# Kernel optimization log

Hardware: AMD Instinct MI355X
Metric: run time of the kernel (lower is better)

## Reference

```python
import jax, jax.numpy as jnp
import numpy as np

B, S, D = 2, 2048, 512
H, DK, DV = 8, 64, 64
TEMP = DK ** 0.5


def setup_inputs() -> dict:
    key = jax.random.key(0)
    ks = jax.random.split(key, 12)
    inp = {
        "q": jax.random.normal(ks[0], (B, S, D), dtype=jnp.float32),
        "k": jax.random.normal(ks[1], (B, S, D), dtype=jnp.float32),
        "v": jax.random.normal(ks[2], (B, S, D), dtype=jnp.float32),
        "static_cov": jax.random.normal(ks[3], (B, S, S), dtype=jnp.float32),
        "mask": jax.random.randint(ks[4], (B, S, S), 0, 2, dtype=jnp.int32),
        # learned params (torch Linear(bias=False) weight is [out,in]; we store [in,out])
        "w_q": jax.random.normal(ks[5], (D, H * DK), dtype=jnp.float32) / np.sqrt(D),
        "w_k": jax.random.normal(ks[6], (D, H * DK), dtype=jnp.float32) / np.sqrt(D),
        "w_v": jax.random.normal(ks[7], (D, H * DV), dtype=jnp.float32) / np.sqrt(D),
        "w_fc": jax.random.normal(ks[8], (H * DV, D), dtype=jnp.float32) / np.sqrt(H * DV),
        "lambda_w": 10.0 * jnp.ones((1, H, 1, 1), dtype=jnp.float32),
        "ln_gamma": jnp.ones((D,), dtype=jnp.float32),
        "ln_beta": jnp.zeros((D,), dtype=jnp.float32),
    }
    return inp


def reference(q, k, v, static_cov, mask, w_q, w_k, w_v, w_fc, lambda_w, ln_gamma, ln_beta):
    residual = q
    # LayerNorm(eps=1e-6) on q only
    mu = jnp.mean(q, axis=-1, keepdims=True)
    var = jnp.mean(jnp.square(q - mu), axis=-1, keepdims=True)
    qn = (q - mu) / jnp.sqrt(var + 1e-6) * ln_gamma + ln_beta
    # projections -> [B, H, S, d]
    qh = (qn @ w_q).reshape(B, S, H, DK).transpose(0, 2, 1, 3)
    kh = (k @ w_k).reshape(B, S, H, DK).transpose(0, 2, 1, 3)
    vh = (v @ w_v).reshape(B, S, H, DV).transpose(0, 2, 1, 3)
    # convex blend of QK^T and static bias
    scores = jnp.einsum('bhqd,bhkd->bhqk', qh / TEMP, kh)  # [B,H,S,S]
    attn = scores / (lambda_w + 1.0) + (lambda_w / (lambda_w + 1.0)) * static_cov[:, None]
    attn = jnp.where(mask[:, None] == 0, -1e9, attn)
    attn = jax.nn.softmax(attn, axis=-1)
    out = jnp.einsum('bhqk,bhkd->bhqd', attn, vh)
    out = out.transpose(0, 2, 1, 3).reshape(B, S, H * DV)
    out = out @ w_fc + residual
    return (out, attn)
```

## Files before the change

kernel.cpp:

```cpp
#include <hip/hip_runtime.h>
#include <hip/hip_bf16.h>

typedef __attribute__((ext_vector_type(4))) float f32x4;
typedef __attribute__((ext_vector_type(4))) int i32x4;
typedef __attribute__((ext_vector_type(4))) unsigned int u32x4;
typedef __attribute__((ext_vector_type(8))) __bf16 bf16x8;

#define SDIM 2048
#define DDIM 512
#define HH 8
#define DH 64

static __device__ __forceinline__ f32x4 mfma_raw(bf16x8 a, bf16x8 b, f32x4 c) {
  return __builtin_amdgcn_mfma_f32_16x16x32_bf16(a, b, c, 0, 0, 0);
}

template <bool C1>
static __device__ __forceinline__ f32x4 mf(bf16x8 a, bf16x8 b, f32x4 c) {
  return C1 ? mfma_raw(a, b, c) : mfma_raw(b, a, c);
}

static __device__ __forceinline__ unsigned pack_bf16(float a, float b) {
  __bf16 x = (__bf16)a, y = (__bf16)b;
  unsigned short ux = __builtin_bit_cast(unsigned short, x);
  unsigned short uy = __builtin_bit_cast(unsigned short, y);
  return ((unsigned)uy << 16) | (unsigned)ux;
}

__global__ __launch_bounds__(256) void covm_kernel(const float* __restrict__ cov,
                                                   const int* __restrict__ mask,
                                                   float* __restrict__ covm,
                                                   int* __restrict__ flag) {
  if (blockIdx.x == 0 && threadIdx.x < 64) {
    float av = (float)(threadIdx.x & 15);
    float bv = av * av;
    bf16x8 a, b;
#pragma unroll
    for (int i = 0; i < 8; ++i) { a[i] = (__bf16)av; b[i] = (__bf16)bv; }
    f32x4 d = {};
    d = mfma_raw(a, b, d);
    if (threadIdx.x == 17) *flag = (d[0] == 128.0f) ? 1 : 2;
  }
  size_t i = ((size_t)blockIdx.x * 256 + threadIdx.x) * 4;
  f32x4 c = *(const f32x4*)(cov + i);
  i32x4 m = *(const i32x4*)(mask + i);
  f32x4 o;
#pragma unroll
  for (int r = 0; r < 4; ++r) o[r] = (m[r] == 0) ? -1e38f : c[r];
  *(f32x4*)(covm + i) = o;
}

__global__ __launch_bounds__(256) void ln_kernel(const float* __restrict__ q,
                                                 const float* __restrict__ gamma,
                                                 const float* __restrict__ beta,
                                                 __bf16* __restrict__ qn) {
  int row = blockIdx.x * 4 + (threadIdx.x >> 6);
  int lane = threadIdx.x & 63;
  const float* qr = q + (size_t)row * DDIM + lane * 8;
  f32x4 x0 = *(const f32x4*)qr;
  f32x4 x1 = *(const f32x4*)(qr + 4);
  float s = 0.f;
#pragma unroll
  for (int i = 0; i < 4; ++i) s += x0[i] + x1[i];
#pragma unroll
  for (int off = 32; off; off >>= 1) s += __shfl_xor(s, off);
  float mu = s * (1.f / DDIM);
  float vs = 0.f;
#pragma unroll
  for (int i = 0; i < 4; ++i) {
    float d0 = x0[i] - mu, d1 = x1[i] - mu;
    vs += d0 * d0 + d1 * d1;
  }
#pragma unroll
  for (int off = 32; off; off >>= 1) vs += __shfl_xor(vs, off);
  float inv = rsqrtf(vs * (1.f / DDIM) + 1e-6f);
  const float* g = gamma + lane * 8;
  const float* be = beta + lane * 8;
  bf16x8 o;
#pragma unroll
  for (int i = 0; i < 8; ++i) {
    float xv = (i < 4) ? x0[i] : x1[i - 4];
    o[i] = (__bf16)((xv - mu) * inv * g[i] + be[i]);
  }
  *(bf16x8*)(qn + (size_t)row * DDIM + lane * 8) = o;
}

__global__ __launch_bounds__(256) void wtrans_kernel(const float* __restrict__ w0,
                                                     const float* __restrict__ w1,
                                                     const float* __restrict__ w2,
                                                     const float* __restrict__ w3,
                                                     __bf16* __restrict__ t0,
                                                     __bf16* __restrict__ t1,
                                                     __bf16* __restrict__ t2,
                                                     __bf16* __restrict__ t3) {
  __shared__ float tile[64][65];
  const float* w = blockIdx.z == 0 ? w0 : blockIdx.z == 1 ? w1 : blockIdx.z == 2 ? w2 : w3;
  __bf16* t = blockIdx.z == 0 ? t0 : blockIdx.z == 1 ? t1 : blockIdx.z == 2 ? t2 : t3;
  int k0 = blockIdx.y * 64;
  int n0 = blockIdx.x * 64;
  int tx = threadIdx.x & 63, ty = threadIdx.x >> 6;
#pragma unroll
  for (int j = 0; j < 16; ++j) {
    int kk = ty * 16 + j;
    tile[kk][tx] = w[(size_t)(k0 + kk) * DDIM + n0 + tx];
  }
  __syncthreads();
#pragma unroll
  for (int j = 0; j < 16; ++j) {
    int n = ty * 16 + j;
    t[(size_t)(n0 + n) * DDIM + k0 + tx] = (__bf16)tile[tx][n];
  }
}

template <bool C1>
static __device__ __forceinline__ void proj_body(const __bf16* __restrict__ qn,
                                                 const float* __restrict__ kin,
                                                 const float* __restrict__ vin,
                                                 const __bf16* __restrict__ wqT,
                                                 const __bf16* __restrict__ wkT,
                                                 const __bf16* __restrict__ wvT,
                                                 const float* __restrict__ lam,
                                                 __bf16* __restrict__ qh,
                                                 __bf16* __restrict__ kh,
                                                 __bf16* __restrict__ vT,
                                                 __bf16* __restrict__ tr) {
  int which = blockIdx.z;
  int n0 = blockIdx.x * 64;
  int m0 = blockIdx.y * 64;
  int wid = threadIdx.x >> 6, lane = threadIdx.x & 63;
  int lr = lane & 15, lg = lane >> 4;
  int mrow = m0 + wid * 16;
  const __bf16* wT = which == 0 ? wqT : which == 1 ? wkT : wvT;
  f32x4 acc[4] = {};
  for (int kb = 0; kb < DDIM; kb += 32) {
    bf16x8 afrag;
    if (which == 0) {
      afrag = *(const bf16x8*)(qn + (size_t)(mrow + lr) * DDIM + kb + lg * 8);
    } else {
      const float* src = (which == 1 ? kin : vin) + (size_t)(mrow + lr) * DDIM + kb + lg * 8;
      f32x4 y0 = *(const f32x4*)src;
      f32x4 y1 = *(const f32x4*)(src + 4);
#pragma unroll
      for (int i = 0; i < 4; ++i) { afrag[i] = (__bf16)y0[i]; afrag[i + 4] = (__bf16)y1[i]; }
    }
#pragma unroll
    for (int c = 0; c < 4; ++c) {
      bf16x8 bfrag = *(const bf16x8*)(wT + (size_t)(n0 + c * 16 + lr) * DDIM + kb + lg * 8);
      acc[c] = mf<C1>(afrag, bfrag, acc[c]);
    }
  }
  int h = n0 >> 6;
  int bq = m0 >> 11;
  int ss0 = m0 & 2047;
  if (which == 0) {
    float sc = 1.f / (8.f * (lam[h] + 1.f));
#pragma unroll
    for (int c = 0; c < 4; ++c)
#pragma unroll
      for (int r = 0; r < 4; ++r)
        tr[(wid * 16 + lg * 4 + r) * 72 + c * 16 + lr] = (__bf16)(acc[c][r] * sc);
  } else if (which == 1) {
#pragma unroll
    for (int c = 0; c < 4; ++c)
#pragma unroll
      for (int r = 0; r < 4; ++r)
        tr[(wid * 16 + lg * 4 + r) * 72 + c * 16 + lr] = (__bf16)acc[c][r];
  } else {
#pragma unroll
    for (int c = 0; c < 4; ++c)
#pragma unroll
      for (int r = 0; r < 4; ++r)
        tr[(c * 16 + lr) * 72 + wid * 16 + lg * 4 + r] = (__bf16)acc[c][r];
  }
  __syncthreads();
  size_t bh2 = (size_t)bq * HH + h;
#pragma unroll
  for (int ii = 0; ii < 2; ++ii) {
    int row = (threadIdx.x >> 3) + ii * 32;
    int col = (threadIdx.x & 7) * 8;
    bf16x8 v8 = *(const bf16x8*)(tr + row * 72 + col);
    if (which == 2) {
      *(bf16x8*)(vT + (bh2 * DH + row) * SDIM + ss0 + col) = v8;
    } else {
      __bf16* dst = (which == 0 ? qh : kh);
      *(bf16x8*)(dst + (bh2 * SDIM + ss0 + row) * DH + col) = v8;
    }
  }
}

__global__ __launch_bounds__(256) void proj_kernel(const __bf16* __restrict__ qn,
                                                   const float* __restrict__ kin,
                                                   const float* __restrict__ vin,
                                                   const __bf16* __restrict__ wqT,
                                                   const __bf16* __restrict__ wkT,
                                                   const __bf16* __restrict__ wvT,
                                                   const float* __restrict__ lam,
                                                   __bf16* __restrict__ qh,
                                                   __bf16* __restrict__ kh,
                                                   __bf16* __restrict__ vT,
                                                   const int* __restrict__ flag) {
  extern __shared__ __bf16 psm[];
  if (*flag == 1) proj_body<true>(qn, kin, vin, wqT, wkT, wvT, lam, qh, kh, vT, psm);
  else            proj_body<false>(qn, kin, vin, wqT, wkT, wvT, lam, qh, kh, vT, psm);
}

template <bool C1>
static __device__ __forceinline__ void fused_body(const __bf16* __restrict__ qh,
                                                  const __bf16* __restrict__ kh,
                                                  const __bf16* __restrict__ vT,
                                                  const float* __restrict__ covm,
                                                  const float* __restrict__ lam,
                                                  float* __restrict__ attn,
                                                  __bf16* __restrict__ oh,
                                                  float* __restrict__ smem) {
  float* part  = smem;
  float* wredm = smem + 16 * 64 * 17;
  float* wreds = wredm + 256;
  int bid = blockIdx.x;
  int xcd = bid & 7;
  int seq = bid >> 3;
  int bh  = xcd * 2 + (seq & 1);
  int q0  = (seq >> 1) * 16;
  int b = bh >> 3, h = bh & 7;
  int wid = threadIdx.x >> 6, lane = threadIdx.x & 63;
  int lr = lane & 15, lg = lane >> 4;
  int col0 = wid * 128;
  const __bf16* qbase = qh + ((size_t)bh * SDIM + q0) * DH;
  const __bf16* kbase = kh + (size_t)bh * SDIM * DH;
  bf16x8 qf0 = *(const bf16x8*)(qbase + lr * DH + lg * 8);
  bf16x8 qf1 = *(const bf16x8*)(qbase + lr * DH + 32 + lg * 8);
  f32x4 acc[8];
#pragma unroll
  for (int c = 0; c < 8; ++c) {
    const __bf16* kp = kbase + (size_t)(col0 + c * 16 + lr) * DH + lg * 8;
    bf16x8 k0 = *(const bf16x8*)kp;
    bf16x8 k1 = *(const bf16x8*)(kp + 32);
    f32x4 t = {};
    t = mf<C1>(k0, qf0, t);
    t = mf<C1>(k1, qf1, t);
    acc[c] = t;
  }
  float blend = lam[h] / (lam[h] + 1.f);
  const float* crow = covm + ((size_t)b * SDIM + q0 + lr) * SDIM + col0 + lg * 4;
  float mx = -3.4e38f;
#pragma unroll
  for (int c = 0; c < 8; ++c) {
    f32x4 cv = *(const f32x4*)(crow + c * 16);
#pragma unroll
    for (int r = 0; r < 4; ++r) {
      float valv = acc[c][r] + blend * cv[r];
      valv = (cv[r] < -1e30f) ? -1e9f : valv;
      acc[c][r] = valv;
      mx = fmaxf(mx, valv);
    }
  }
  mx = fmaxf(mx, __shfl_xor(mx, 16));
  mx = fmaxf(mx, __shfl_xor(mx, 32));
  if (lg == 0) wredm[wid * 16 + lr] = mx;
  __syncthreads();
  float fm = wredm[lr];
#pragma unroll
  for (int w = 1; w < 16; ++w) fm = fmaxf(fm, wredm[w * 16 + lr]);
  float sm = 0.f;
#pragma unroll
  for (int c = 0; c < 8; ++c) {
#pragma unroll
    for (int r = 0; r < 4; ++r) {
      float p = __expf(acc[c][r] - fm);
      acc[c][r] = p;
      sm += p;
    }
  }
  sm += __shfl_xor(sm, 16);
  sm += __shfl_xor(sm, 32);
  if (lg == 0) wreds[wid * 16 + lr] = sm;
  __syncthreads();
  float ssum = wreds[lr];
#pragma unroll
  for (int w = 1; w < 16; ++w) ssum += wreds[w * 16 + lr];
  float inv = 1.f / ssum;
  unsigned pw[8][2];
#pragma unroll
  for (int c = 0; c < 8; ++c) {
    pw[c][0] = pack_bf16(acc[c][0] * inv, acc[c][1] * inv);
    pw[c][1] = pack_bf16(acc[c][2] * inv, acc[c][3] * inv);
  }
  const __bf16* vbase = vT + (size_t)bh * DH * SDIM + col0;
  int src0 = lr + 32 * (lg & 1);
  int src1 = src0 + 16;
  bool hi = (lg & 2) != 0;
  f32x4 oacc[4] = {};
#pragma unroll
  for (int t = 0; t < 4; ++t) {
    unsigned a0 = (unsigned)__shfl((int)pw[t * 2][0], src0);
    unsigned a1 = (unsigned)__shfl((int)pw[t * 2][1], src0);
    unsigned b0 = (unsigned)__shfl((int)pw[t * 2 + 1][0], src0);
    unsigned b1 = (unsigned)__shfl((int)pw[t * 2 + 1][1], src0);
    unsigned a2 = (unsigned)__shfl((int)pw[t * 2][0], src1);
    unsigned a3 = (unsigned)__shfl((int)pw[t * 2][1], src1);
    unsigned b2 = (unsigned)__shfl((int)pw[t * 2 + 1][0], src1);
    unsigned b3 = (unsigned)__shfl((int)pw[t * 2 + 1][1], src1);
    u32x4 wv;
    wv[0] = hi ? b0 : a0;
    wv[1] = hi ? b1 : a1;
    wv[2] = hi ? b2 : a2;
    wv[3] = hi ? b3 : a3;
    bf16x8 pfrag = __builtin_bit_cast(bf16x8, wv);
#pragma unroll
    for (int cp = 0; cp < 4; ++cp) {
      bf16x8 vfrag = *(const bf16x8*)(vbase + (size_t)(cp * 16 + lr) * SDIM + t * 32 + lg * 8);
      oacc[cp] = mf<C1>(vfrag, pfrag, oacc[cp]);
    }
  }
#pragma unroll
  for (int cp = 0; cp < 4; ++cp)
#pragma unroll
    for (int rp = 0; rp < 4; ++rp)
      part[(wid * 64 + cp * 16 + lg * 4 + rp) * 17 + lr] = oacc[cp][rp];
  __syncthreads();
  float* abase = attn + ((size_t)bh * SDIM + q0 + lr) * SDIM + col0 + lg * 4;
#pragma unroll
  for (int c = 0; c < 8; ++c) {
    f32x4 pn;
#pragma unroll
    for (int r = 0; r < 4; ++r) pn[r] = acc[c][r] * inv;
    *(f32x4*)(abase + c * 16) = pn;
  }
  {
    int qq = threadIdx.x >> 6;
    int dv = threadIdx.x & 63;
    float s = 0.f;
#pragma unroll
    for (int w = 0; w < 16; ++w) s += part[(w * 64 + dv) * 17 + qq];
    float sn = __shfl_xor(s, 1);
    if ((dv & 1) == 0) {
      unsigned ow = pack_bf16(s, sn);
      *(unsigned*)(oh + ((size_t)(b * SDIM + q0 + qq)) * DDIM + h * DH + dv) = ow;
    }
  }
}

__global__ __launch_bounds__(1024, 4) void fused_kernel_cov(const __bf16* __restrict__ qh,
                                                            const __bf16* __restrict__ kh,
                                                            const __bf16* __restrict__ vT,
                                                            const float* __restrict__ covm,
                                                            const float* __restrict__ lam,
                                                            float* __restrict__ attn,
                                                            __bf16* __restrict__ oh,
                                                            const int* __restrict__ flag) {
  extern __shared__ float smem[];
  if (*flag == 1) fused_body<true>(qh, kh, vT, covm, lam, attn, oh, smem);
  else            fused_body<false>(qh, kh, vT, covm, lam, attn, oh, smem);
}

template <bool C1>
static __device__ __forceinline__ void fc_body(const __bf16* __restrict__ oh,
                                               const __bf16* __restrict__ wfcT,
                                               const float* __restrict__ resid,
                                               float* __restrict__ out) {
  int n0 = blockIdx.x * 64;
  int m0 = blockIdx.y * 64;
  int wid = threadIdx.x >> 6, lane = threadIdx.x & 63;
  int lr = lane & 15, lg = lane >> 4;
  int mrow = m0 + wid * 16;
  f32x4 acc[4] = {};
  for (int kb = 0; kb < DDIM; kb += 32) {
    bf16x8 afrag = *(const bf16x8*)(oh + (size_t)(mrow + lr) * DDIM + kb + lg * 8);
#pragma unroll
    for (int c = 0; c < 4; ++c) {
      bf16x8 bfrag = *(const bf16x8*)(wfcT + (size_t)(n0 + c * 16 + lr) * DDIM + kb + lg * 8);
      acc[c] = mf<C1>(afrag, bfrag, acc[c]);
    }
  }
#pragma unroll
  for (int c = 0; c < 4; ++c)
#pragma unroll
    for (int r = 0; r < 4; ++r) {
      size_t m = mrow + lg * 4 + r;
      size_t n = n0 + c * 16 + lr;
      out[m * DDIM + n] = acc[c][r] + resid[m * DDIM + n];
    }
}

__global__ __launch_bounds__(256) void fc_kernel(const __bf16* __restrict__ oh,
                                                 const __bf16* __restrict__ wfcT,
                                                 const float* __restrict__ resid,
                                                 float* __restrict__ out,
                                                 const int* __restrict__ flag) {
  if (*flag == 1) fc_body<true>(oh, wfcT, resid, out);
  else            fc_body<false>(oh, wfcT, resid, out);
}

extern "C" void kernel_launch(void* const* d_in, const int* in_sizes, int n_in,
                              void* d_out, int out_size, void* d_ws, size_t ws_size,
                              hipStream_t stream) {
  const float* q = (const float*)d_in[0];
  const float* k = (const float*)d_in[1];
  const float* v = (const float*)d_in[2];
  const float* static_cov = (const float*)d_in[3];
  const int* mask = (const int*)d_in[4];
  const float* w_q = (const float*)d_in[5];
  const float* w_k = (const float*)d_in[6];
  const float* w_v = (const float*)d_in[7];
  const float* w_fc = (const float*)d_in[8];
  const float* lam = (const float*)d_in[9];
  const float* gamma = (const float*)d_in[10];
  const float* beta = (const float*)d_in[11];

  float* out = (float*)d_out;
  float* attn = out + (size_t)2 * SDIM * DDIM;

  char* ws = (char*)d_ws;
  const size_t MB4 = (size_t)4 << 20;
  __bf16* qn  = (__bf16*)(ws);
  __bf16* qh  = (__bf16*)(ws + 1 * MB4);
  __bf16* kh  = (__bf16*)(ws + 2 * MB4);
  __bf16* vT  = (__bf16*)(ws + 3 * MB4);
  __bf16* oh  = (__bf16*)(ws + 4 * MB4);
  __bf16* wqT = (__bf16*)(ws + 5 * MB4);
  __bf16* wkT = (__bf16*)(ws + 5 * MB4 + 524288);
  __bf16* wvT = (__bf16*)(ws + 5 * MB4 + 2 * 524288);
  __bf16* wfcT= (__bf16*)(ws + 5 * MB4 + 3 * 524288);
  int* flag   = (int*)(ws + 5 * MB4 + 4 * 524288);
  float* covm = (float*)(ws + 6 * MB4);

  const unsigned fused_smem = (16 * 64 * 17 + 256 + 256) * 4;
  const unsigned proj_smem  = 64 * 72 * 2;

  covm_kernel<<<dim3(2 * SDIM * SDIM / 1024), dim3(256), 0, stream>>>(static_cov, mask, covm, flag);
  ln_kernel<<<dim3(1024), dim3(256), 0, stream>>>(q, gamma, beta, qn);
  wtrans_kernel<<<dim3(8, 8, 4), dim3(256), 0, stream>>>(w_q, w_k, w_v, w_fc, wqT, wkT, wvT, wfcT);
  proj_kernel<<<dim3(8, 64, 3), dim3(256), proj_smem, stream>>>(qn, k, v, wqT, wkT, wvT, lam, qh, kh, vT, flag);
  fused_kernel_cov<<<dim3(2048), dim3(1024), fused_smem, stream>>>(qh, kh, vT, covm, lam, attn, oh, flag);
  fc_kernel<<<dim3(8, 64), dim3(256), 0, stream>>>(oh, wfcT, q, out, flag);
}
```

Before: 318.6 us.

## Merge prep kernels into one launch and use single-barrier softmax reduction

Result: faster. 311.5 us (-2.2%).

```diff
diff --git a/kernel.cpp b/kernel.cpp
--- a/kernel.cpp
+++ b/kernel.cpp
@@ -27,77 +27,84 @@
   return ((unsigned)uy << 16) | (unsigned)ux;
 }
 
-__global__ __launch_bounds__(256) void covm_kernel(const float* __restrict__ cov,
-                                                   const int* __restrict__ mask,
-                                                   float* __restrict__ covm,
-                                                   int* __restrict__ flag) {
-  if (blockIdx.x == 0 && threadIdx.x < 64) {
-    float av = (float)(threadIdx.x & 15);
-    float bv = av * av;
-    bf16x8 a, b;
-#pragma unroll
-    for (int i = 0; i < 8; ++i) { a[i] = (__bf16)av; b[i] = (__bf16)bv; }
-    f32x4 d = {};
-    d = mfma_raw(a, b, d);
-    if (threadIdx.x == 17) *flag = (d[0] == 128.0f) ? 1 : 2;
-  }
-  size_t i = ((size_t)blockIdx.x * 256 + threadIdx.x) * 4;
-  f32x4 c = *(const f32x4*)(cov + i);
-  i32x4 m = *(const i32x4*)(mask + i);
-  f32x4 o;
-#pragma unroll
-  for (int r = 0; r < 4; ++r) o[r] = (m[r] == 0) ? -1e38f : c[r];
-  *(f32x4*)(covm + i) = o;
-}
-
-__global__ __launch_bounds__(256) void ln_kernel(const float* __restrict__ q,
-                                                 const float* __restrict__ gamma,
-                                                 const float* __restrict__ beta,
-                                                 __bf16* __restrict__ qn) {
-  int row = blockIdx.x * 4 + (threadIdx.x >> 6);
-  int lane = threadIdx.x & 63;
-  const float* qr = q + (size_t)row * DDIM + lane * 8;
-  f32x4 x0 = *(const f32x4*)qr;
-  f32x4 x1 = *(const f32x4*)(qr + 4);
-  float s = 0.f;
-#pragma unroll
-  for (int i = 0; i < 4; ++i) s += x0[i] + x1[i];
-#pragma unroll
-  for (int off = 32; off; off >>= 1) s += __shfl_xor(s, off);
-  float mu = s * (1.f / DDIM);
-  float vs = 0.f;
-#pragma unroll
-  for (int i = 0; i < 4; ++i) {
-    float d0 = x0[i] - mu, d1 = x1[i] - mu;
-    vs += d0 * d0 + d1 * d1;
-  }
-#pragma unroll
-  for (int off = 32; off; off >>= 1) vs += __shfl_xor(vs, off);
-  float inv = rsqrtf(vs * (1.f / DDIM) + 1e-6f);
-  const float* g = gamma + lane * 8;
-  const float* be = beta + lane * 8;
-  bf16x8 o;
-#pragma unroll
-  for (int i = 0; i < 8; ++i) {
-    float xv = (i < 4) ? x0[i] : x1[i - 4];
-    o[i] = (__bf16)((xv - mu) * inv * g[i] + be[i]);
-  }
-  *(bf16x8*)(qn + (size_t)row * DDIM + lane * 8) = o;
-}
-
-__global__ __launch_bounds__(256) void wtrans_kernel(const float* __restrict__ w0,
+__global__ __launch_bounds__(256) void stageA_kernel(const float* __restrict__ cov,
+                                                     const int* __restrict__ mask,
+                                                     float* __restrict__ covm,
+                                                     const float* __restrict__ q,
+                                                     const float* __restrict__ gamma,
+                                                     const float* __restrict__ beta,
+                                                     __bf16* __restrict__ qn,
+                                                     const float* __restrict__ w0,
                                                      const float* __restrict__ w1,
                                                      const float* __restrict__ w2,
                                                      const float* __restrict__ w3,
                                                      __bf16* __restrict__ t0,
                                                      __bf16* __restrict__ t1,
                                                      __bf16* __restrict__ t2,
-                                                     __bf16* __restrict__ t3) {
+                                                     __bf16* __restrict__ t3,
+                                                     int* __restrict__ flag) {
   __shared__ float tile[64][65];
-  const float* w = blockIdx.z == 0 ? w0 : blockIdx.z == 1 ? w1 : blockIdx.z == 2 ? w2 : w3;
-  __bf16* t = blockIdx.z == 0 ? t0 : blockIdx.z == 1 ? t1 : blockIdx.z == 2 ? t2 : t3;
-  int k0 = blockIdx.y * 64;
-  int n0 = blockIdx.x * 64;
+  int bid = blockIdx.x;
+  if (bid < 8192) {
+    size_t i = ((size_t)bid * 256 + threadIdx.x) * 4;
+    f32x4 c = *(const f32x4*)(cov + i);
+    i32x4 m = *(const i32x4*)(mask + i);
+    f32x4 o;
+#pragma unroll
+    for (int r = 0; r < 4; ++r) o[r] = (m[r] == 0) ? -1e38f : c[r];
+    *(f32x4*)(covm + i) = o;
+    return;
+  }
+  if (bid < 9216) {
+    int lb = bid - 8192;
+    if (lb == 0 && threadIdx.x < 64) {
+      float av = (float)(threadIdx.x & 15);
+      float bv = av * av;
+      bf16x8 a, b;
+#pragma unroll
+      for (int i = 0; i < 8; ++i) { a[i] = (__bf16)av; b[i] = (__bf16)bv; }
+      f32x4 d = {};
+      d = mfma_raw(a, b, d);
+      if (threadIdx.x == 17) *flag = (d[0] == 128.0f) ? 1 : 2;
+    }
+    int row = lb * 4 + (threadIdx.x >> 6);
+    int lane = threadIdx.x & 63;
+    const float* qr = q + (size_t)row * DDIM + lane * 8;
+    f32x4 x0 = *(const f32x4*)qr;
+    f32x4 x1 = *(const f32x4*)(qr + 4);
+    float s = 0.f;
+#pragma unroll
+    for (int i = 0; i < 4; ++i) s += x0[i] + x1[i];
+#pragma unroll
+    for (int off = 32; off; off >>= 1) s += __shfl_xor(s, off);
+    float mu = s * (1.f / DDIM);
+    float vs = 0.f;
+#pragma unroll
+    for (int i = 0; i < 4; ++i) {
+      float d0 = x0[i] - mu, d1 = x1[i] - mu;
+      vs += d0 * d0 + d1 * d1;
+    }
+#pragma unroll
+    for (int off = 32; off; off >>= 1) vs += __shfl_xor(vs, off);
+    float inv = rsqrtf(vs * (1.f / DDIM) + 1e-6f);
+    const float* g = gamma + lane * 8;
+    const float* be = beta + lane * 8;
+    bf16x8 o;
+#pragma unroll
+    for (int i = 0; i < 8; ++i) {
+      float xv = (i < 4) ? x0[i] : x1[i - 4];
+      o[i] = (__bf16)((xv - mu) * inv * g[i] + be[i]);
+    }
+    *(bf16x8*)(qn + (size_t)row * DDIM + lane * 8) = o;
+    return;
+  }
+  int wb = bid - 9216;
+  int which = wb >> 6;
+  int rem = wb & 63;
+  int n0 = (rem & 7) * 64;
+  int k0 = (rem >> 3) * 64;
+  const float* w = which == 0 ? w0 : which == 1 ? w1 : which == 2 ? w2 : w3;
+  __bf16* t = which == 0 ? t0 : which == 1 ? t1 : which == 2 ? t2 : t3;
   int tx = threadIdx.x & 63, ty = threadIdx.x >> 6;
 #pragma unroll
   for (int j = 0; j < 16; ++j) {
@@ -256,34 +263,35 @@
   }
   mx = fmaxf(mx, __shfl_xor(mx, 16));
   mx = fmaxf(mx, __shfl_xor(mx, 32));
-  if (lg == 0) wredm[wid * 16 + lr] = mx;
-  __syncthreads();
-  float fm = wredm[lr];
-#pragma unroll
-  for (int w = 1; w < 16; ++w) fm = fmaxf(fm, wredm[w * 16 + lr]);
   float sm = 0.f;
 #pragma unroll
   for (int c = 0; c < 8; ++c) {
 #pragma unroll
     for (int r = 0; r < 4; ++r) {
-      float p = __expf(acc[c][r] - fm);
+      float p = __expf(acc[c][r] - mx);
       acc[c][r] = p;
       sm += p;
     }
   }
   sm += __shfl_xor(sm, 16);
   sm += __shfl_xor(sm, 32);
-  if (lg == 0) wreds[wid * 16 + lr] = sm;
+  if (lg == 0) {
+    wredm[wid * 16 + lr] = mx;
+    wreds[wid * 16 + lr] = sm;
+  }
   __syncthreads();
-  float ssum = wreds[lr];
-#pragma unroll
-  for (int w = 1; w < 16; ++w) ssum += wreds[w * 16 + lr];
-  float inv = 1.f / ssum;
+  float M = wredm[lr];
+#pragma unroll
+  for (int w = 1; w < 16; ++w) M = fmaxf(M, wredm[w * 16 + lr]);
+  float denom = 0.f;
+#pragma unroll
+  for (int w = 0; w < 16; ++w) denom += wreds[w * 16 + lr] * __expf(wredm[w * 16 + lr] - M);
+  float sc = __expf(mx - M) / denom;
   unsigned pw[8][2];
 #pragma unroll
   for (int c = 0; c < 8; ++c) {
-    pw[c][0] = pack_bf16(acc[c][0] * inv, acc[c][1] * inv);
-    pw[c][1] = pack_bf16(acc[c][2] * inv, acc[c][3] * inv);
+    pw[c][0] = pack_bf16(acc[c][0] * sc, acc[c][1] * sc);
+    pw[c][1] = pack_bf16(acc[c][2] * sc, acc[c][3] * sc);
   }
   const __bf16* vbase = vT + (size_t)bh * DH * SDIM + col0;
   int src0 = lr + 32 * (lg & 1);
@@ -323,7 +331,7 @@
   for (int c = 0; c < 8; ++c) {
     f32x4 pn;
 #pragma unroll
-    for (int r = 0; r < 4; ++r) pn[r] = acc[c][r] * inv;
+    for (int r = 0; r < 4; ++r) pn[r] = acc[c][r] * sc;
     *(f32x4*)(abase + c * 16) = pn;
   }
   {
@@ -427,9 +435,10 @@
   const unsigned fused_smem = (16 * 64 * 17 + 256 + 256) * 4;
   const unsigned proj_smem  = 64 * 72 * 2;
 
-  covm_kernel<<<dim3(2 * SDIM * SDIM / 1024), dim3(256), 0, stream>>>(static_cov, mask, covm, flag);
-  ln_kernel<<<dim3(1024), dim3(256), 0, stream>>>(q, gamma, beta, qn);
-  wtrans_kernel<<<dim3(8, 8, 4), dim3(256), 0, stream>>>(w_q, w_k, w_v, w_fc, wqT, wkT, wvT, wfcT);
+  stageA_kernel<<<dim3(9472), dim3(256), 0, stream>>>(static_cov, mask, covm,
+                                                      q, gamma, beta, qn,
+                                                      w_q, w_k, w_v, w_fc,
+                                                      wqT, wkT, wvT, wfcT, flag);
   proj_kernel<<<dim3(8, 64, 3), dim3(256), proj_smem, stream>>>(qn, k, v, wqT, wkT, wvT, lam, qh, kh, vT, flag);
   fused_kernel_cov<<<dim3(2048), dim3(1024), fused_smem, stream>>>(qh, kh, vT, covm, lam, attn, oh, flag);
   fc_kernel<<<dim3(8, 64), dim3(256), 0, stream>>>(oh, wfcT, q, out, flag);
```
